# Performance work log

Measured on AMD Instinct MI355X. Metric: run time of the kernel, lower is better.

The kernel has to match this reference:

```python
import jax, jax.numpy as jnp
import numpy as np

B, C, H, W = 8, 256, 64, 64
NUM_LABELS = 16  # labels in {-1, 0..15}; -1 means 'no group'


def setup_inputs() -> dict:
    key = jax.random.key(0)
    kx, kl, kw, kb = jax.random.split(key, 4)
    x = jax.random.normal(kx, (B, C, H, W), dtype=jnp.float32)
    # labels in [-1, NUM_LABELS)
    labels = jax.random.randint(kl, (B * C,), 0, NUM_LABELS + 1) - 1
    # groups=C, kernel 1x1: conv weight is (3C,1,1,1) -> per-output-channel scale; bias (3C,)
    w = jax.random.normal(kw, (3 * C,), dtype=jnp.float32) * 0.5
    b = jax.random.normal(kb, (3 * C,), dtype=jnp.float32) * 0.02
    return {"x": x, "labels": labels, "w": w, "b": b}


def reference(x, labels, w, b):
    # x: (B,C,h,w); labels: (B*C,); w,b: (3C,)
    Bv, Cv, hv, wv = x.shape
    hw = hv * wv
    xf = x.reshape(Bv, Cv, hw)
    # grouped 1x1 conv: out channel o (of 3C) reads input channel o//3
    x_rep = jnp.repeat(xf, 3, axis=1)                      # (B,3C,hw)
    qkv = x_rep * w[None, :, None] + b[None, :, None]      # (B,3C,hw)
    flat = qkv.reshape(Bv * 3 * Cv, hw)                    # matches torch reshape(1,3BC,hw)
    BC = Bv * Cv
    q, k, v = flat[:BC], flat[BC:2 * BC], flat[2 * BC:]    # each (BC, hw)
    valid = labels != -1                                   # (BC,)
    same = (labels[:, None] == labels[None, :]) & valid[:, None] & valid[None, :]
    # per-label-group attention == masked dense attention (softmax over same-label cols only)
    scores = q @ k.T                                       # (BC, BC), no sqrt(d) scaling (as in source)
    neg = jnp.finfo(scores.dtype).min
    scores = jnp.where(same, scores, neg)
    weights = jax.nn.softmax(scores, axis=-1)
    out = weights @ v                                      # (BC, hw)
    out = jnp.where(valid[:, None], out, jnp.zeros((), out.dtype))  # -1 rows stay zero
    return out[None]                                       # (1, BC, hw)
```

## Files before the change

### kernel.cpp

```cpp
#include <hip/hip_runtime.h>
#include <cfloat>

#define B_   8
#define C_   256
#define HW_  4096
#define BC_  2048
#define TC_  768
#define NG_  16
#define MAXG 320
#define UK0  682
#define NUQ  683
#define NUK  684
#define NXU  1366
#define NXALL 2048

#define SPLITK 8
#define NT     11
#define NTILES (NT * NT)
#define KSL    (HW_ / SPLITK)
#define WKC    (KSL / 4)
#define NP1    (NUQ * NUK)
#define REDBLK ((NP1 / 4 + 255) / 256)

#define MCAP  192
#define CST   192
#define BKP   216

typedef __attribute__((ext_vector_type(8))) short short8;
typedef __attribute__((ext_vector_type(4))) float floatx4;

__device__ __forceinline__ unsigned short f32_to_bf16_rne(float f) {
  unsigned u = __float_as_uint(f);
  unsigned r = (u + 0x7FFFu + ((u >> 16) & 1u)) >> 16;
  return (unsigned short)r;
}

__global__ __launch_bounds__(256) void prep_kernel(
    const float* __restrict__ x, const int* __restrict__ labels,
    unsigned short* __restrict__ xhi, unsigned short* __restrict__ xlo,
    float* __restrict__ sums, int* __restrict__ grp_n,
    int* __restrict__ members, int* __restrict__ posArr, int nhi)
{
  const int t = threadIdx.x;
  if (blockIdx.x < NG_) {
    __shared__ int lab[BC_];
    __shared__ int cnts[256];
    const int g = blockIdx.x;
    for (int idx = t; idx < BC_; idx += 256) lab[idx] = labels[idx];
    __syncthreads();
    const int base = t * 8;
    int cnt = 0;
#pragma unroll
    for (int k = 0; k < 8; k++) cnt += (lab[base + k] == g) ? 1 : 0;
    cnts[t] = cnt;
    for (int off = 1; off < 256; off <<= 1) {
      __syncthreads();
      const int v = (t >= off) ? cnts[t - off] : 0;
      __syncthreads();
      cnts[t] += v;
    }
    __syncthreads();
    int pos = cnts[t] - cnt;
    if (t == 255) grp_n[g] = cnts[255] < MAXG ? cnts[255] : MAXG;
#pragma unroll
    for (int k = 0; k < 8; k++) {
      const int i = base + k;
      if (lab[i] == g) {
        if (pos < MAXG) { members[g * MAXG + pos] = i; posArr[i] = pos; }
        pos++;
      }
    }
    return;
  }

  const int u = blockIdx.x - NG_;
  const float* row = x + (size_t)u * HW_;
  unsigned short* hrow = xhi + (size_t)u * HW_;
  if (u < NXU) {
    unsigned short* lrow = xlo + (size_t)u * HW_;
    float s = 0.f;
#pragma unroll
    for (int i = 0; i < 4; i++) {
      const int col = i * 1024 + t * 4;
      const float4 v = *(const float4*)(row + col);
      s += v.x + v.y + v.z + v.w;
      ushort4 h, l;
      h.x = f32_to_bf16_rne(v.x);
      h.y = f32_to_bf16_rne(v.y);
      h.z = f32_to_bf16_rne(v.z);
      h.w = f32_to_bf16_rne(v.w);
      l.x = f32_to_bf16_rne(v.x - __uint_as_float((unsigned)h.x << 16));
      l.y = f32_to_bf16_rne(v.y - __uint_as_float((unsigned)h.y << 16));
      l.z = f32_to_bf16_rne(v.z - __uint_as_float((unsigned)h.z << 16));
      l.w = f32_to_bf16_rne(v.w - __uint_as_float((unsigned)h.w << 16));
      *(ushort4*)(hrow + col) = h;
      *(ushort4*)(lrow + col) = l;
    }
#pragma unroll
    for (int o = 32; o > 0; o >>= 1) s += __shfl_down(s, o);
    __shared__ float red[4];
    if ((t & 63) == 0) red[t >> 6] = s;
    __syncthreads();
    if (t == 0) sums[u] = red[0] + red[1] + red[2] + red[3];
  } else {
#pragma unroll
    for (int i = 0; i < 4; i++) {
      const int col = i * 1024 + t * 4;
      const float4 v = *(const float4*)(row + col);
      ushort4 h;
      h.x = f32_to_bf16_rne(v.x);
      h.y = f32_to_bf16_rne(v.y);
      h.z = f32_to_bf16_rne(v.z);
      h.w = f32_to_bf16_rne(v.w);
      *(ushort4*)(hrow + col) = h;
    }
  }
}

__global__ __launch_bounds__(256) void gram_mfma_kernel(
    const unsigned short* __restrict__ xhi, const unsigned short* __restrict__ xlo,
    float* __restrict__ P)
{
  const int bid  = blockIdx.x;
  const int z    = bid & 7;
  const int tile = bid >> 3;
  const int m0 = (tile % NT) * 64;
  const int n0 = (tile / NT) * 64;

  const int t = threadIdx.x;
  const int wave = t >> 6;
  const int lane = t & 63;
  const int fr = lane & 15;
  const int fq = lane >> 4;

  const int kbase = z * KSL + wave * WKC + fq * 8;
  const unsigned short *pah[4], *pal[4], *pbh[4], *pbl[4];
#pragma unroll
  for (int i = 0; i < 4; i++) {
    const int ar = min(m0 + fr + i * 16, NUQ - 1);
    const int br = min(UK0 + n0 + fr + i * 16, NXU - 1);
    pah[i] = xhi + (size_t)ar * HW_ + kbase;
    pal[i] = xlo + (size_t)ar * HW_ + kbase;
    pbh[i] = xhi + (size_t)br * HW_ + kbase;
    pbl[i] = xlo + (size_t)br * HW_ + kbase;
  }

  floatx4 acc[4][4];
#pragma unroll
  for (int i = 0; i < 4; i++)
#pragma unroll
    for (int j = 0; j < 4; j++) acc[i][j] = (floatx4)(0.f);

  for (int kk = 0; kk < WKC; kk += 32) {
    short8 ah[4], al[4], bh[4], bl[4];
#pragma unroll
    for (int i = 0; i < 4; i++) {
      ah[i] = *(const short8*)(pah[i] + kk);
      al[i] = *(const short8*)(pal[i] + kk);
      bh[i] = *(const short8*)(pbh[i] + kk);
      bl[i] = *(const short8*)(pbl[i] + kk);
    }
#pragma unroll
    for (int mt = 0; mt < 4; mt++)
#pragma unroll
      for (int nt = 0; nt < 4; nt++) {
        acc[mt][nt] = __builtin_amdgcn_mfma_f32_16x16x32_bf16(ah[mt], bh[nt], acc[mt][nt], 0, 0, 0);
        acc[mt][nt] = __builtin_amdgcn_mfma_f32_16x16x32_bf16(al[mt], bh[nt], acc[mt][nt], 0, 0, 0);
        acc[mt][nt] = __builtin_amdgcn_mfma_f32_16x16x32_bf16(ah[mt], bl[nt], acc[mt][nt], 0, 0, 0);
      }
  }

  __shared__ float R[2][64][68];
  float* R0 = &R[0][0][0];
  float* R1 = &R[1][0][0];
  if (wave == 0 || wave == 2) {
    float* Rw = (wave == 0) ? R0 : R1;
#pragma unroll
    for (int mt = 0; mt < 4; mt++)
#pragma unroll
      for (int nt = 0; nt < 4; nt++)
#pragma unroll
        for (int r = 0; r < 4; r++)
          Rw[(mt * 16 + fq * 4 + r) * 68 + nt * 16 + fr] = acc[mt][nt][r];
  }
  __syncthreads();
  if (wave == 1 || wave == 3) {
    float* Rw = (wave == 1) ? R0 : R1;
#pragma unroll
    for (int mt = 0; mt < 4; mt++)
#pragma unroll
      for (int nt = 0; nt < 4; nt++)
#pragma unroll
        for (int r = 0; r < 4; r++)
          Rw[(mt * 16 + fq * 4 + r) * 68 + nt * 16 + fr] += acc[mt][nt][r];
  }
  __syncthreads();
  const int em = t >> 2;
  const int en = (t & 3) * 16;
  const int gm = m0 + em;
  if (gm < NUQ) {
    float* dst = P + (size_t)z * NP1 + (size_t)gm * NUK + n0;
#pragma unroll
    for (int i4 = 0; i4 < 4; i4++) {
      const int n = en + i4 * 4;
      if (n0 + n < NUK) {
        float4 v;
        v.x = R0[em * 68 + n + 0] + R1[em * 68 + n + 0];
        v.y = R0[em * 68 + n + 1] + R1[em * 68 + n + 1];
        v.z = R0[em * 68 + n + 2] + R1[em * 68 + n + 2];
        v.w = R0[em * 68 + n + 3] + R1[em * 68 + n + 3];
        *(float4*)(dst + n) = v;
      }
    }
  }
}

__global__ __launch_bounds__(256) void reduce_tab_kernel(
    const float* __restrict__ P, float* __restrict__ S,
    const float* __restrict__ w, const float* __restrict__ bbias,
    const float* __restrict__ sums, const int* __restrict__ grp_n,
    const int* __restrict__ members, float4* __restrict__ gtA,
    float2* __restrict__ gtB)
{
  const int bid = blockIdx.x;
  const int t = threadIdx.x;
  if (bid < REDBLK) {
    const int idx = (bid * 256 + t) * 4;
    if (idx < NP1) {
      float4 s = *(const float4*)(P + idx);
#pragma unroll
      for (int sl = 1; sl < SPLITK; sl++) {
        const float4 a = *(const float4*)(P + (size_t)sl * NP1 + idx);
        s.x += a.x; s.y += a.y; s.z += a.z; s.w += a.w;
      }
      *(float4*)(S + idx) = s;
    }
    return;
  }
  const int g = bid - REDBLK;
  const int n = grp_n[g];
  for (int p = t; p < n; p += 256) {
    const int j = members[g * MAXG + p];
    const int rk = j + BC_;
    const int jk = rk % TC_;
    const int uk = (rk / TC_) * C_ + jk / 3;
    const int jv = (j + 2 * BC_) % TC_;
    gtA[g * MAXG + p] = make_float4(w[jk], bbias[jk], sums[uk], w[jv]);
    gtB[g * MAXG + p] = make_float2(bbias[jv], __int_as_float(uk - UK0));
  }
}

__device__ __forceinline__ float blockReduceMax(float v, float* red) {
#pragma unroll
  for (int o = 32; o > 0; o >>= 1) v = fmaxf(v, __shfl_down(v, o));
  if ((threadIdx.x & 63) == 0) red[threadIdx.x >> 6] = v;
  __syncthreads();
  v = fmaxf(fmaxf(red[0], red[1]), fmaxf(red[2], red[3]));
  __syncthreads();
  return v;
}
__device__ __forceinline__ float blockReduceSum(float v, float* red) {
#pragma unroll
  for (int o = 32; o > 0; o >>= 1) v += __shfl_down(v, o);
  if ((threadIdx.x & 63) == 0) red[threadIdx.x >> 6] = v;
  __syncthreads();
  v = red[0] + red[1] + red[2] + red[3];
  __syncthreads();
  return v;
}

__global__ __launch_bounds__(256) void softmax_kernel(
    const int* __restrict__ labels, const float* __restrict__ w,
    const float* __restrict__ bbias, const float* __restrict__ sums,
    const float* __restrict__ S, const int* __restrict__ grp_n,
    const int* __restrict__ posArr, const float4* __restrict__ gtA,
    const float2* __restrict__ gtB, unsigned short* __restrict__ coefh,
    float* __restrict__ cb, float* __restrict__ out)
{
  const int i = blockIdx.x;
  const int t = threadIdx.x;
  const int g = labels[i];
  if (g < 0) {
    const float4 z = make_float4(0.f, 0.f, 0.f, 0.f);
    float4* orow = (float4*)(out + (size_t)i * HW_);
    for (int cidx = t; cidx < HW_ / 4; cidx += 256) orow[cidx] = z;
    return;
  }
  __shared__ float red[4];
  const int n   = grp_n[g];
  const int jq  = i % TC_;
  const int uqi = (i / TC_) * C_ + jq / 3;
  const float wq = w[jq], bq = bbias[jq];
  const float sq = sums[uqi];
  const float* Srow = S + (size_t)uqi * NUK;

  const int jj0 = t, jj1 = t + 256;
  float4 A0, A1; float2 B0, B1;
  float s0 = -FLT_MAX, s1 = -FLT_MAX;
  if (jj0 < n) {
    A0 = gtA[g * MAXG + jj0];
    B0 = gtB[g * MAXG + jj0];
    s0 = wq * A0.x * Srow[__float_as_int(B0.y)] + (wq * A0.y) * sq +
         (bq * A0.x) * A0.z + (bq * A0.y) * 4096.f;
  }
  if (jj1 < n) {
    A1 = gtA[g * MAXG + jj1];
    B1 = gtB[g * MAXG + jj1];
    s1 = wq * A1.x * Srow[__float_as_int(B1.y)] + (wq * A1.y) * sq +
         (bq * A1.x) * A1.z + (bq * A1.y) * 4096.f;
  }
  const float mx = blockReduceMax(fmaxf(s0, s1), red);
  const float e0 = (jj0 < n) ? expf(s0 - mx) : 0.f;
  const float e1 = (jj1 < n) ? expf(s1 - mx) : 0.f;
  const float tot = blockReduceSum(e0 + e1, red);
  const float inv = 1.f / tot;

  const int pos = posArr[i];
  unsigned short* crow = coefh + ((size_t)g * MCAP + pos) * CST;
  float lcb = 0.f;
  if (jj0 < n) {
    const float wgt = e0 * inv;
    if (pos < MCAP && jj0 < CST) crow[jj0] = f32_to_bf16_rne(wgt * A0.w);
    lcb += wgt * B0.x;
  } else if (pos < MCAP && jj0 < CST) {
    crow[jj0] = 0;
  }
  if (jj1 < n) {
    const float wgt = e1 * inv;
    lcb += wgt * B1.x;
  }
  const float cbi = blockReduceSum(lcb, red);
  if (t == 0) cb[i] = cbi;
}

__global__ __launch_bounds__(256) void out_mfma_kernel(
    const float* __restrict__ x, const unsigned short* __restrict__ xh,
    const unsigned short* __restrict__ coefh,
    const float* __restrict__ cb, const int* __restrict__ grp_n,
    const int* __restrict__ members, float* __restrict__ out)
{
  const int g  = blockIdx.x;
  const int c0 = blockIdx.y * 64;
  const int n  = min(grp_n[g], MCAP);
  if (n == 0) return;
  const int Kceil = (n + 31) & ~31;
  const int nk8 = Kceil >> 3;
  const int t = threadIdx.x;
  const int wave = t >> 6;
  const int lane = t & 63;
  const int fr = lane & 15;
  const int fq = lane >> 4;

  __shared__ unsigned short Bt[64][BKP];
  __shared__ int   mem[MCAP];
  __shared__ float cbs[MCAP];

  if (t < n) {
    const int j = members[g * MAXG + t];
    mem[t] = j;
    cbs[t] = cb[j];
  }
  __syncthreads();

  {
    const int colq = t & 15;
    const int kcb  = t >> 4;
    for (int kc = kcb; kc < nk8; kc += 16) {
      if (xh) {
        ushort4 hv[8];
#pragma unroll
        for (int j = 0; j < 8; j++) {
          const int k = kc * 8 + j;
          if (k < n) {
            const int jm = mem[k];
            const int rv = jm + 2 * BC_;
            const int uv = (rv / TC_) * C_ + (rv % TC_) / 3;
            hv[j] = *(const ushort4*)(xh + (size_t)uv * HW_ + c0 + colq * 4);
          } else {
            hv[j] = make_ushort4(0, 0, 0, 0);
          }
        }
#pragma unroll
        for (int c = 0; c < 4; c++) {
          short8 pk;
          pk[0] = (short)(c == 0 ? hv[0].x : c == 1 ? hv[0].y : c == 2 ? hv[0].z : hv[0].w);
          pk[1] = (short)(c == 0 ? hv[1].x : c == 1 ? hv[1].y : c == 2 ? hv[1].z : hv[1].w);
          pk[2] = (short)(c == 0 ? hv[2].x : c == 1 ? hv[2].y : c == 2 ? hv[2].z : hv[2].w);
          pk[3] = (short)(c == 0 ? hv[3].x : c == 1 ? hv[3].y : c == 2 ? hv[3].z : hv[3].w);
          pk[4] = (short)(c == 0 ? hv[4].x : c == 1 ? hv[4].y : c == 2 ? hv[4].z : hv[4].w);
          pk[5] = (short)(c == 0 ? hv[5].x : c == 1 ? hv[5].y : c == 2 ? hv[5].z : hv[5].w);
          pk[6] = (short)(c == 0 ? hv[6].x : c == 1 ? hv[6].y : c == 2 ? hv[6].z : hv[6].w);
          pk[7] = (short)(c == 0 ? hv[7].x : c == 1 ? hv[7].y : c == 2 ? hv[7].z : hv[7].w);
          *(short8*)&Bt[colq * 4 + c][kc * 8] = pk;
        }
      } else {
        float4 vals[8];
#pragma unroll
        for (int j = 0; j < 8; j++) {
          const int k = kc * 8 + j;
          if (k < n) {
            const int jm = mem[k];
            const int rv = jm + 2 * BC_;
            const int uv = (rv / TC_) * C_ + (rv % TC_) / 3;
            vals[j] = *(const float4*)(x + (size_t)uv * HW_ + c0 + colq * 4);
          } else {
            vals[j] = make_float4(0.f, 0.f, 0.f, 0.f);
          }
        }
#pragma unroll
        for (int c = 0; c < 4; c++) {
          short8 pk;
          pk[0] = (short)f32_to_bf16_rne(c == 0 ? vals[0].x : c == 1 ? vals[0].y : c == 2 ? vals[0].z : vals[0].w);
          pk[1] = (short)f32_to_bf16_rne(c == 0 ? vals[1].x : c == 1 ? vals[1].y : c == 2 ? vals[1].z : vals[1].w);
          pk[2] = (short)f32_to_bf16_rne(c == 0 ? vals[2].x : c == 1 ? vals[2].y : c == 2 ? vals[2].z : vals[2].w);
          pk[3] = (short)f32_to_bf16_rne(c == 0 ? vals[3].x : c == 1 ? vals[3].y : c == 2 ? vals[3].z : vals[3].w);
          pk[4] = (short)f32_to_bf16_rne(c == 0 ? vals[4].x : c == 1 ? vals[4].y : c == 2 ? vals[4].z : vals[4].w);
          pk[5] = (short)f32_to_bf16_rne(c == 0 ? vals[5].x : c == 1 ? vals[5].y : c == 2 ? vals[5].z : vals[5].w);
          pk[6] = (short)f32_to_bf16_rne(c == 0 ? vals[6].x : c == 1 ? vals[6].y : c == 2 ? vals[6].z : vals[6].w);
          pk[7] = (short)f32_to_bf16_rne(c == 0 ? vals[7].x : c == 1 ? vals[7].y : c == 2 ? vals[7].z : vals[7].w);
          *(short8*)&Bt[colq * 4 + c][kc * 8] = pk;
        }
      }
    }
  }
  __syncthreads();

  const int colw = wave * 16 + fr;

  for (int m0 = 0; m0 < n; m0 += 32) {
    floatx4 acc0 = (floatx4)(0.f), acc1 = (floatx4)(0.f);
    const unsigned short* pa0 = coefh + ((size_t)g * MCAP + m0 + fr) * CST + fq * 8;
    const unsigned short* pa1 = pa0 + 16 * CST;
    for (int k = 0; k < Kceil; k += 32) {
      const short8 a0 = *(const short8*)(pa0 + k);
      const short8 a1 = *(const short8*)(pa1 + k);
      const short8 b  = *(const short8*)&Bt[colw][fq * 8 + k];
      acc0 = __builtin_amdgcn_mfma_f32_16x16x32_bf16(a0, b, acc0, 0, 0, 0);
      acc1 = __builtin_amdgcn_mfma_f32_16x16x32_bf16(a1, b, acc1, 0, 0, 0);
    }
#pragma unroll
    for (int r = 0; r < 4; r++) {
      int m = m0 + fq * 4 + r;
      if (m < n) out[(size_t)mem[m] * HW_ + c0 + colw] = acc0[r] + cbs[m];
      m += 16;
      if (m < n) out[(size_t)mem[m] * HW_ + c0 + colw] = acc1[r] + cbs[m];
    }
  }
}

extern "C" void kernel_launch(void* const* d_in, const int* in_sizes, int n_in,
                              void* d_out, int out_size, void* d_ws, size_t ws_size,
                              hipStream_t stream)
{
  const float* x      = (const float*)d_in[0];
  const int*   labels = (const int*)d_in[1];
  const float* w      = (const float*)d_in[2];
  const float* bb     = (const float*)d_in[3];
  float* out = (float*)d_out;

  char* wsb = (char*)d_ws;
  size_t off = 0;
  auto carve = [&](size_t bytes) -> void* {
    off = (off + 255) & ~(size_t)255;
    void* p = wsb + off;
    off += bytes;
    return p;
  };
  float* sums    = (float*)carve(NXU * sizeof(float));
  float* S       = (float*)carve((size_t)NP1 * sizeof(float));
  float* P       = (float*)carve((size_t)SPLITK * NP1 * sizeof(float));
  int*   grp_n   = (int*)carve(NG_ * sizeof(int));
  int*   members = (int*)carve((size_t)NG_ * MAXG * sizeof(int));
  int*   posArr  = (int*)carve(BC_ * sizeof(int));
  unsigned short* coefh = (unsigned short*)carve((size_t)NG_ * MCAP * CST * sizeof(unsigned short));
  float* cb      = (float*)carve(BC_ * sizeof(float));
  float4* gtA    = (float4*)carve((size_t)NG_ * MAXG * sizeof(float4));
  float2* gtB    = (float2*)carve((size_t)NG_ * MAXG * sizeof(float2));

  const int big = ws_size >= (size_t)47 * 1024 * 1024;
  const int nhi = big ? NXALL : NXU;
  unsigned short* xhi = (unsigned short*)carve((size_t)nhi * HW_ * sizeof(unsigned short));
  unsigned short* xlo = (unsigned short*)carve((size_t)NXU * HW_ * sizeof(unsigned short));

  prep_kernel<<<NG_ + nhi, 256, 0, stream>>>(x, labels, xhi, xlo, sums,
                                             grp_n, members, posArr, nhi);
  gram_mfma_kernel<<<NTILES * SPLITK, 256, 0, stream>>>(xhi, xlo, P);
  reduce_tab_kernel<<<REDBLK + NG_, 256, 0, stream>>>(P, S, w, bb, sums,
                                                      grp_n, members, gtA, gtB);
  softmax_kernel<<<BC_, 256, 0, stream>>>(labels, w, bb, sums, S, grp_n,
                                          posArr, gtA, gtB, coefh, cb, out);
  out_mfma_kernel<<<dim3(NG_, HW_ / 64), 256, 0, stream>>>(
      x, big ? xhi : (const unsigned short*)nullptr, coefh, cb, grp_n,
      members, out);
}
```

Measured before the change: 162.1 us.

## Fuse split-K reduction and gather table into gram kernel via last-block atomic

Removes the separate reduce_tab kernel. Each gram tile's split-K blocks increment a per-tile atomic counter, and the last block to arrive sums the eight partial slices into S. The per-group gather-table construction moves into the z==0 blocks of the first 16 tiles, and prep_kernel zeroes the counters. This saves one kernel launch and its tail, in exchange for thread fences, an atomic per block, and serialized reduction work on the last-arriving blocks.

```diff
diff --git a/kernel.cpp b/kernel.cpp
--- a/kernel.cpp
+++ b/kernel.cpp
@@ -20,7 +20,6 @@
 #define KSL    (HW_ / SPLITK)
 #define WKC    (KSL / 4)
 #define NP1    (NUQ * NUK)
-#define REDBLK ((NP1 / 4 + 255) / 256)
 
 #define MCAP  192
 #define CST   192
@@ -39,10 +38,12 @@
     const float* __restrict__ x, const int* __restrict__ labels,
     unsigned short* __restrict__ xhi, unsigned short* __restrict__ xlo,
     float* __restrict__ sums, int* __restrict__ grp_n,
-    int* __restrict__ members, int* __restrict__ posArr, int nhi)
+    int* __restrict__ members, int* __restrict__ posArr,
+    int* __restrict__ tilecnt, int nhi)
 {
   const int t = threadIdx.x;
   if (blockIdx.x < NG_) {
+    if (blockIdx.x == 0 && t < NTILES) tilecnt[t] = 0;
     __shared__ int lab[BC_];
     __shared__ int cnts[256];
     const int g = blockIdx.x;
@@ -119,7 +120,11 @@
 
 __global__ __launch_bounds__(256) void gram_mfma_kernel(
     const unsigned short* __restrict__ xhi, const unsigned short* __restrict__ xlo,
-    float* __restrict__ P)
+    float* __restrict__ P, float* __restrict__ S, int* __restrict__ tilecnt,
+    const float* __restrict__ w, const float* __restrict__ bbias,
+    const float* __restrict__ sums, const int* __restrict__ grp_n,
+    const int* __restrict__ members, float4* __restrict__ gtA,
+    float2* __restrict__ gtB)
 {
   const int bid  = blockIdx.x;
   const int z    = bid & 7;
@@ -132,6 +137,20 @@
   const int lane = t & 63;
   const int fr = lane & 15;
   const int fq = lane >> 4;
+
+  if (z == 0 && tile < NG_) {
+    const int g = tile;
+    const int n = grp_n[g];
+    for (int p = t; p < n; p += 256) {
+      const int j = members[g * MAXG + p];
+      const int rk = j + BC_;
+      const int jk = rk % TC_;
+      const int uk = (rk / TC_) * C_ + jk / 3;
+      const int jv = (j + 2 * BC_) % TC_;
+      gtA[g * MAXG + p] = make_float4(w[jk], bbias[jk], sums[uk], w[jv]);
+      gtB[g * MAXG + p] = make_float2(bbias[jv], __int_as_float(uk - UK0));
+    }
+  }
 
   const int kbase = z * KSL + wave * WKC + fq * 8;
   const unsigned short *pah[4], *pal[4], *pbh[4], *pbl[4];
@@ -213,40 +232,30 @@
       }
     }
   }
-}
-
-__global__ __launch_bounds__(256) void reduce_tab_kernel(
-    const float* __restrict__ P, float* __restrict__ S,
-    const float* __restrict__ w, const float* __restrict__ bbias,
-    const float* __restrict__ sums, const int* __restrict__ grp_n,
-    const int* __restrict__ members, float4* __restrict__ gtA,
-    float2* __restrict__ gtB)
-{
-  const int bid = blockIdx.x;
-  const int t = threadIdx.x;
-  if (bid < REDBLK) {
-    const int idx = (bid * 256 + t) * 4;
-    if (idx < NP1) {
-      float4 s = *(const float4*)(P + idx);
-#pragma unroll
-      for (int sl = 1; sl < SPLITK; sl++) {
-        const float4 a = *(const float4*)(P + (size_t)sl * NP1 + idx);
-        s.x += a.x; s.y += a.y; s.z += a.z; s.w += a.w;
+
+  __threadfence();
+  __shared__ int lastFlag;
+  if (t == 0)
+    lastFlag = (atomicAdd(&tilecnt[tile], 1) == SPLITK - 1) ? 1 : 0;
+  __syncthreads();
+  if (lastFlag) {
+    __threadfence();
+    if (gm < NUQ) {
+      const size_t rowoff = (size_t)gm * NUK + n0;
+#pragma unroll
+      for (int i4 = 0; i4 < 4; i4++) {
+        const int n = en + i4 * 4;
+        if (n0 + n < NUK) {
+          float4 s = *(const float4*)(P + rowoff + n);
+#pragma unroll
+          for (int sl = 1; sl < SPLITK; sl++) {
+            const float4 a = *(const float4*)(P + (size_t)sl * NP1 + rowoff + n);
+            s.x += a.x; s.y += a.y; s.z += a.z; s.w += a.w;
+          }
+          *(float4*)(S + rowoff + n) = s;
+        }
       }
-      *(float4*)(S + idx) = s;
-    }
-    return;
-  }
-  const int g = bid - REDBLK;
-  const int n = grp_n[g];
-  for (int p = t; p < n; p += 256) {
-    const int j = members[g * MAXG + p];
-    const int rk = j + BC_;
-    const int jk = rk % TC_;
-    const int uk = (rk / TC_) * C_ + jk / 3;
-    const int jv = (j + 2 * BC_) % TC_;
-    gtA[g * MAXG + p] = make_float4(w[jk], bbias[jk], sums[uk], w[jv]);
-    gtB[g * MAXG + p] = make_float2(bbias[jv], __int_as_float(uk - UK0));
+    }
   }
 }
 
@@ -472,6 +481,7 @@
   int*   grp_n   = (int*)carve(NG_ * sizeof(int));
   int*   members = (int*)carve((size_t)NG_ * MAXG * sizeof(int));
   int*   posArr  = (int*)carve(BC_ * sizeof(int));
+  int*   tilecnt = (int*)carve(NTILES * sizeof(int));
   unsigned short* coefh = (unsigned short*)carve((size_t)NG_ * MCAP * CST * sizeof(unsigned short));
   float* cb      = (float*)carve(BC_ * sizeof(float));
   float4* gtA    = (float4*)carve((size_t)NG_ * MAXG * sizeof(float4));
@@ -483,10 +493,9 @@
   unsigned short* xlo = (unsigned short*)carve((size_t)NXU * HW_ * sizeof(unsigned short));
 
   prep_kernel<<<NG_ + nhi, 256, 0, stream>>>(x, labels, xhi, xlo, sums,
-                                             grp_n, members, posArr, nhi);
-  gram_mfma_kernel<<<NTILES * SPLITK, 256, 0, stream>>>(xhi, xlo, P);
-  reduce_tab_kernel<<<REDBLK + NG_, 256, 0, stream>>>(P, S, w, bb, sums,
-                                                      grp_n, members, gtA, gtB);
+                                             grp_n, members, posArr, tilecnt, nhi);
+  gram_mfma_kernel<<<NTILES * SPLITK, 256, 0, stream>>>(
+      xhi, xlo, P, S, tilecnt, w, bb, sums, grp_n, members, gtA, gtB);
   softmax_kernel<<<BC_, 256, 0, stream>>>(labels, w, bb, sums, S, grp_n,
                                           posArr, gtA, gtB, coefh, cb, out);
   out_mfma_kernel<<<dim3(NG_, HW_ / 64), 256, 0, stream>>>(
```

Result: slower. 430.0 us (+165.3%).
